# Performance work log

Measured on AMD Instinct MI355X. Metric: run time of the kernel, lower is better.

The kernel has to match this reference:

```python
import jax, jax.numpy as jnp
import numpy as np

N, D_IN, D_OUT, H, E = 8192, 1024, 1024, 1024, 8
EPS = 0.2
S_FACTOR = 5.0


def setup_inputs() -> dict:
    key = jax.random.key(0)
    k0, k1, k2, k3 = jax.random.split(key, 4)
    x = jax.random.normal(k0, (N, D_IN), jnp.float32)
    # selector Linear(nIn, E); weights scaled by sFactor as in SMoE.__init__
    Wsel = jax.random.normal(k1, (D_IN, E), jnp.float32) * (S_FACTOR / np.sqrt(D_IN))
    bsel = jnp.zeros((E,), jnp.float32)
    # stacked 2-layer MLP experts: Linear(D_IN,H) -> ReLU -> Linear(H,D_OUT)
    W1 = jax.random.normal(k2, (E, D_IN, H), jnp.float32) / np.sqrt(D_IN)
    b1 = jnp.zeros((E, H), jnp.float32)
    W2 = jax.random.normal(k3, (E, H, D_OUT), jnp.float32) / np.sqrt(H)
    b2 = jnp.zeros((E, D_OUT), jnp.float32)
    return {"x": x, "Wsel": Wsel, "bsel": bsel, "W1": W1, "b1": b1, "W2": W2, "b2": b2}


def _sparse_weights(weightMat):
    # sort experts per token, descending (torch.sort(..., 1, descending=True))
    order = jnp.argsort(-weightMat, axis=1)                # [N,E]
    topW = jnp.take_along_axis(weightMat, order, axis=1)
    cumW = jnp.cumsum(topW, axis=1)
    capped = jnp.minimum(cumW, 1.0 - EPS)
    sw_sorted = jax.nn.relu(capped - cumW + topW)          # sparse weights, sorted order
    # softCost (side-effect metric in the original; not returned by SMoE.forward)
    shifted = jnp.pad(sw_sorted[:, 1:], ((0, 0), (0, 1)))
    _soft_cost = jnp.sum(jnp.where(shifted > 0, 1.0, sw_sorted), axis=1)
    # faithful to torch.gather(sparse_weight, 1, index) in the source
    sw = jnp.take_along_axis(sw_sorted, order, axis=1)     # [N,E]
    return sw


def reference(x, Wsel, bsel, W1, b1, W2, b2):
    weightMat = jax.nn.softmax(x @ Wsel + bsel, axis=1)    # [N,E] selector
    sw = _sparse_weights(weightMat)                        # [N,E] sparse combine weights
    # dense (vectorized) expert dispatch: tokens with sw==0 contribute 0,
    # numerically identical to the gather/scatter_add loop in sparse_MoE
    h = jax.nn.relu(jnp.einsum('nd,edh->enh', x, W1) + b1[:, None, :])   # [E,N,H]
    y = jnp.einsum('enh,eho->eno', h, W2) + b2[:, None, :]               # [E,N,O]
    out = jnp.einsum('ne,eno->no', sw, y)                                # [N,O]
    return out
```

## Files before the change

kernel.cpp:

```cpp
#include <hip/hip_runtime.h>
#include <hip/hip_bf16.h>
#include <stdint.h>

#define N_TOK 8192
#define DIN   1024
#define DOUT  1024
#define HID   1024
#define NE    8
#define CAP   0.8f

typedef __attribute__((ext_vector_type(8))) short short8;
typedef __attribute__((ext_vector_type(4))) float floatx4;

__device__ __forceinline__ void async_load16(const void* g, void* l) {
  __builtin_amdgcn_global_load_lds(
      (const __attribute__((address_space(1))) void*)g,
      (__attribute__((address_space(3))) void*)l,
      16, 0, 0);
}

__device__ __forceinline__ unsigned short bf16_bits(float f) {
  return __builtin_bit_cast(unsigned short, __float2bfloat16(f));
}

__global__ __launch_bounds__(256) void selector_kernel(
    const float* __restrict__ x, const float* __restrict__ Wsel,
    const float* __restrict__ bsel,
    __hip_bfloat16* __restrict__ x_bf, float* __restrict__ sw,
    float4* __restrict__ out4)
{
  {
    const int base = blockIdx.x * 1024 + threadIdx.x;
    const float4 z4 = {0.f, 0.f, 0.f, 0.f};
#pragma unroll
    for (int r = 0; r < 4; r++) out4[base + r * 256] = z4;
  }

  const int lane = threadIdx.x & 63;
  const int wave = threadIdx.x >> 6;
  const int n = blockIdx.x * 4 + wave;
  const float4* xr4 = (const float4*)(x + (size_t)n * DIN);
  ushort4* xb4 = (ushort4*)(x_bf + (size_t)n * DIN);

  float acc[8];
#pragma unroll
  for (int e = 0; e < 8; e++) acc[e] = 0.f;

#pragma unroll
  for (int i = 0; i < 4; i++) {
    const int d4 = lane + i * 64;
    const float4 xv = xr4[d4];
    ushort4 p;
    p.x = bf16_bits(xv.x);
    p.y = bf16_bits(xv.y);
    p.z = bf16_bits(xv.z);
    p.w = bf16_bits(xv.w);
    xb4[d4] = p;
    const float xs[4] = {xv.x, xv.y, xv.z, xv.w};
#pragma unroll
    for (int q = 0; q < 4; q++) {
      const int d = d4 * 4 + q;
      const float4* wr = (const float4*)(Wsel + d * 8);
      const float4 wlo = wr[0], whi = wr[1];
      const float xv1 = xs[q];
      acc[0] += xv1 * wlo.x; acc[1] += xv1 * wlo.y;
      acc[2] += xv1 * wlo.z; acc[3] += xv1 * wlo.w;
      acc[4] += xv1 * whi.x; acc[5] += xv1 * whi.y;
      acc[6] += xv1 * whi.z; acc[7] += xv1 * whi.w;
    }
  }
#pragma unroll
  for (int off = 32; off >= 1; off >>= 1)
#pragma unroll
    for (int e = 0; e < 8; e++) acc[e] += __shfl_xor(acc[e], off);

  if (lane == 0) {
    float w[8];
    float mx = -1e30f;
#pragma unroll
    for (int e = 0; e < 8; e++) { w[e] = acc[e] + bsel[e]; mx = fmaxf(mx, w[e]); }
    float s = 0.f;
#pragma unroll
    for (int e = 0; e < 8; e++) { w[e] = expf(w[e] - mx); s += w[e]; }
    const float inv = 1.f / s;
#pragma unroll
    for (int e = 0; e < 8; e++) w[e] *= inv;

    float wsrt[8]; int ord[8];
    for (int k = 0; k < 8; k++) {
      const float v = w[k];
      int j = k;
      while (j > 0 && wsrt[j - 1] < v) { wsrt[j] = wsrt[j - 1]; ord[j] = ord[j - 1]; j--; }
      wsrt[j] = v; ord[j] = k;
    }
    float cum = 0.f, sws[8];
    for (int k = 0; k < 8; k++) {
      cum += wsrt[k];
      const float capped = fminf(cum, CAP);
      sws[k] = fmaxf(capped - cum + wsrt[k], 0.f);
    }
    for (int j = 0; j < 8; j++) sw[(size_t)n * 8 + j] = sws[ord[j]];
  }
}

__global__ __launch_bounds__(256) void compact_convert_kernel(
    const float* __restrict__ sw, int* __restrict__ idx, int* __restrict__ cnt,
    const float* __restrict__ W1, const float* __restrict__ W2,
    __hip_bfloat16* __restrict__ W1t, __hip_bfloat16* __restrict__ W2t)
{
  const int z = blockIdx.z;
  if (z == 16) {
    const int bid = blockIdx.x + 32 * blockIdx.y;
    if (bid >= 8) return;
    const int e = bid;
    const int t = threadIdx.x;
    const int lane = t & 63;
    const int wv = t >> 6;
    __shared__ int wave_base[4];
    __shared__ int chunk_total;
    int base = 0;
    for (int c = 0; c < 32; c++) {
      const int tok = c * 256 + t;
      const bool act = sw[(size_t)tok * 8 + e] > 0.f;
      const unsigned long long m = __ballot(act);
      const int before = __popcll(m & ((1ull << lane) - 1ull));
      if (lane == 0) wave_base[wv] = __popcll(m);
      __syncthreads();
      if (t == 0) {
        int s = 0;
        for (int w = 0; w < 4; w++) { const int v = wave_base[w]; wave_base[w] = s; s += v; }
        chunk_total = s;
      }
      __syncthreads();
      if (act) idx[e * N_TOK + base + wave_base[wv] + before] = tok;
      base += chunk_total;
      __syncthreads();
    }
    if (t == 0) cnt[e] = base;
    return;
  }

  __shared__ float tile[32][33];
  const float* src = (z & 8) ? W2 : W1;
  __hip_bfloat16* dst = (z & 8) ? W2t : W1t;
  const int e = z & 7;
  src += (size_t)e * 1024 * 1024;
  dst += (size_t)e * 1024 * 1024;
  const int R = blockIdx.y * 32, C = blockIdx.x * 32;
  const int c = threadIdx.x & 31, r0 = threadIdx.x >> 5;
#pragma unroll
  for (int p = 0; p < 4; p++) {
    const int r = r0 + p * 8;
    tile[r][c] = src[(size_t)(R + r) * 1024 + C + c];
  }
  __syncthreads();
#pragma unroll
  for (int p = 0; p < 4; p++) {
    const int r = r0 + p * 8;
    dst[(size_t)(C + r) * 1024 + R + c] = __float2bfloat16(tile[c][r]);
  }
}

#define BUFO (128 * 32)

template <int MODE>
__global__ __launch_bounds__(256, 2) void moe_gemm(
    const __hip_bfloat16* __restrict__ x_bf,
    __hip_bfloat16* __restrict__ hpool,
    const __hip_bfloat16* __restrict__ Wt,
    const float* __restrict__ biasAll,
    const float* __restrict__ sw,
    const int* __restrict__ idx, const int* __restrict__ cnt,
    float* __restrict__ out)
{
  const int lid = blockIdx.x + (blockIdx.y << 3) + (blockIdx.z << 9);
  const int xcd = lid & 7;
  const int s_ = lid >> 3;
  const int nb = s_ & 7;
  const int g  = s_ >> 3;
  const int e  = g & 7;
  const int mb = ((xcd - e) & 7) + ((g >> 3) << 3);

  const int count = cnt[e];
  const int m0 = mb * 128;
  if (m0 >= count) return;
  const int n0 = nb * 128;

  __shared__ __align__(16) __hip_bfloat16 sA[2 * BUFO];
  __shared__ __align__(16) __hip_bfloat16 sB[2 * BUFO];
  const int t = threadIdx.x;
  const int lane = t & 63;
  const int wave = t >> 6;
  const int wm = (wave & 1) * 64;
  const int wn = (wave >> 1) * 64;
  const int* idx_e = idx + e * N_TOK;
  const float* bias = biasAll + e * 1024;

  floatx4 acc[4][4];
#pragma unroll
  for (int i = 0; i < 4; i++)
#pragma unroll
    for (int j = 0; j < 4; j++) acc[i][j] = (floatx4){0.f, 0.f, 0.f, 0.f};

  const int sr = t >> 2;
  const int sc = (t & 3) * 8;
  const __hip_bfloat16* Ag0;
  const __hip_bfloat16* Ag1;
  if (MODE == 0) {
    const int t0 = idx_e[min(m0 + sr, count - 1)];
    const int t1 = idx_e[min(m0 + sr + 64, count - 1)];
    Ag0 = x_bf + (size_t)t0 * 1024 + sc;
    Ag1 = x_bf + (size_t)t1 * 1024 + sc;
  } else {
    const __hip_bfloat16* hp = hpool + (size_t)e * N_TOK * 1024;
    Ag0 = hp + (size_t)(m0 + sr) * 1024 + sc;
    Ag1 = hp + (size_t)(m0 + sr + 64) * 1024 + sc;
  }
  const __hip_bfloat16* Bg = Wt + (size_t)e * 1024 * 1024 + (size_t)(n0 + sr) * 1024 + sc;
  __hip_bfloat16* lA = &sA[sr * 32 + sc];
  __hip_bfloat16* lB = &sB[sr * 32 + sc];

  const int rf = lane & 15;
  const int k8 = (lane >> 4) * 8;
  const int roA = (wm + rf) * 32 + k8;
  const int roB = (wn + rf) * 32 + k8;

  async_load16(Ag0, lA);
  async_load16(Ag1, lA + 64 * 32);
  async_load16(Bg, lB);
  async_load16(Bg + (size_t)64 * 1024, lB + 64 * 32);
  __syncthreads();

#define STEP(KT, RB, WB)                                                        \
  {                                                                             \
    const int knext = ((KT) + 1) * 32;                                          \
    if (knext < 1024) {                                                         \
      async_load16(Ag0 + knext, lA + (WB) * BUFO);                              \
      async_load16(Ag1 + knext, lA + (WB) * BUFO + 64 * 32);                    \
      async_load16(Bg + knext, lB + (WB) * BUFO);                               \
      async_load16(Bg + (size_t)64 * 1024 + knext, lB + (WB) * BUFO + 64 * 32); \
    }                                                                           \
    const __hip_bfloat16* pA = &sA[(RB) * BUFO + roA];                          \
    const __hip_bfloat16* pB = &sB[(RB) * BUFO + roB];                          \
    short8 aF[4], bF[4];                                                        \
    _Pragma("unroll")                                                           \
    for (int i = 0; i < 4; i++) aF[i] = *(const short8*)(pA + i * 16 * 32);     \
    _Pragma("unroll")                                                           \
    for (int j = 0; j < 4; j++) bF[j] = *(const short8*)(pB + j * 16 * 32);     \
    _Pragma("unroll")                                                           \
    for (int i = 0; i < 4; i++)                                                 \
      _Pragma("unroll")                                                         \
      for (int j = 0; j < 4; j++)                                               \
        acc[i][j] = __builtin_amdgcn_mfma_f32_16x16x32_bf16(aF[i], bF[j],       \
                                                            acc[i][j], 0, 0, 0);\
    __syncthreads();                                                            \
  }

  for (int kt = 0; kt < 32; kt += 2) {
    STEP(kt, 0, 1);
    STEP(kt + 1, 1, 0);
  }
#undef STEP

  const int quad = lane >> 4;
  const int cn = lane & 15;
#pragma unroll
  for (int i = 0; i < 4; i++) {
#pragma unroll
    for (int r = 0; r < 4; r++) {
      const int gm = m0 + wm + i * 16 + quad * 4 + r;
      if (gm >= count) continue;
      int tok = 0; float swv = 0.f;
      if (MODE == 1) {
        tok = idx_e[gm];
        swv = sw[tok * 8 + e];
      }
#pragma unroll
      for (int j = 0; j < 4; j++) {
        const int gn = n0 + wn + j * 16 + cn;
        const float v = acc[i][j][r] + bias[gn];
        if (MODE == 0) {
          hpool[((size_t)e * N_TOK + gm) * 1024 + gn] = __float2bfloat16(fmaxf(v, 0.f));
        } else {
          unsafeAtomicAdd(&out[(size_t)tok * 1024 + gn], swv * v);
        }
      }
    }
  }
}

extern "C" void kernel_launch(void* const* d_in, const int* in_sizes, int n_in,
                              void* d_out, int out_size, void* d_ws, size_t ws_size,
                              hipStream_t stream) {
  const float* x    = (const float*)d_in[0];
  const float* Wsel = (const float*)d_in[1];
  const float* bsel = (const float*)d_in[2];
  const float* W1   = (const float*)d_in[3];
  const float* b1   = (const float*)d_in[4];
  const float* W2   = (const float*)d_in[5];
  const float* b2   = (const float*)d_in[6];
  float* out = (float*)d_out;

  char* ws = (char*)d_ws;
  __hip_bfloat16* x_bf = (__hip_bfloat16*)ws; ws += (size_t)N_TOK * DIN * 2;
  __hip_bfloat16* W1t  = (__hip_bfloat16*)ws; ws += (size_t)NE * DIN * HID * 2;
  __hip_bfloat16* W2t  = (__hip_bfloat16*)ws; ws += (size_t)NE * HID * DOUT * 2;
  float* sw            = (float*)ws;          ws += (size_t)N_TOK * NE * 4;
  int* idx             = (int*)ws;            ws += (size_t)NE * N_TOK * 4;
  int* cnt             = (int*)ws;            ws += 256;
  __hip_bfloat16* hpool = (__hip_bfloat16*)ws;

  selector_kernel<<<N_TOK / 4, 256, 0, stream>>>(x, Wsel, bsel, x_bf, sw,
                                                 (float4*)out);
  compact_convert_kernel<<<dim3(32, 32, 17), 256, 0, stream>>>(
      sw, idx, cnt, W1, W2, W1t, W2t);

  moe_gemm<0><<<dim3(HID / 128, N_TOK / 128, NE), 256, 0, stream>>>(
      x_bf, hpool, W1t, b1, sw, idx, cnt, out);
  moe_gemm<1><<<dim3(DOUT / 128, N_TOK / 128, NE), 256, 0, stream>>>(
      x_bf, hpool, W2t, b2, sw, idx, cnt, out);
}
```

Measured before the change: 322.0 us.

## Vectorize weight transpose-convert, widen compaction blocks, simplify GEMM block mapping

The weight transpose/convert kernel now uses 64x64 tiles with 1024 threads, float4 loads, and ushort4 bf16 stores, storing bf16 bits in shared memory. This cuts memory transactions and shared-memory traffic. The compaction step now processes 1024 tokens per iteration with 16 wave slots, so it needs fewer barrier rounds. The GEMM block index mapping drops the XCD-aware swizzle for a direct blockIdx mapping, which may hurt L2 locality across XCDs.

```diff
diff --git a/kernel.cpp b/kernel.cpp
--- a/kernel.cpp
+++ b/kernel.cpp
@@ -103,24 +103,26 @@
   }
 }
 
-__global__ __launch_bounds__(256) void compact_convert_kernel(
+__global__ __launch_bounds__(1024) void compact_convert_kernel(
     const float* __restrict__ sw, int* __restrict__ idx, int* __restrict__ cnt,
     const float* __restrict__ W1, const float* __restrict__ W2,
     __hip_bfloat16* __restrict__ W1t, __hip_bfloat16* __restrict__ W2t)
 {
   const int z = blockIdx.z;
+  const int t = threadIdx.x;
+
   if (z == 16) {
-    const int bid = blockIdx.x + 32 * blockIdx.y;
+    const int bid = blockIdx.x + 16 * blockIdx.y;
     if (bid >= 8) return;
     const int e = bid;
-    const int t = threadIdx.x;
     const int lane = t & 63;
     const int wv = t >> 6;
-    __shared__ int wave_base[4];
+    __shared__ int wave_base[16];
     __shared__ int chunk_total;
     int base = 0;
-    for (int c = 0; c < 32; c++) {
-      const int tok = c * 256 + t;
+#pragma unroll
+    for (int c = 0; c < 8; c++) {
+      const int tok = c * 1024 + t;
       const bool act = sw[(size_t)tok * 8 + e] > 0.f;
       const unsigned long long m = __ballot(act);
       const int before = __popcll(m & ((1ull << lane) - 1ull));
@@ -128,7 +130,7 @@
       __syncthreads();
       if (t == 0) {
         int s = 0;
-        for (int w = 0; w < 4; w++) { const int v = wave_base[w]; wave_base[w] = s; s += v; }
+        for (int w = 0; w < 16; w++) { const int v = wave_base[w]; wave_base[w] = s; s += v; }
         chunk_total = s;
       }
       __syncthreads();
@@ -140,24 +142,33 @@
     return;
   }
 
-  __shared__ float tile[32][33];
+  __shared__ unsigned short tile[64][65];
   const float* src = (z & 8) ? W2 : W1;
   __hip_bfloat16* dst = (z & 8) ? W2t : W1t;
   const int e = z & 7;
   src += (size_t)e * 1024 * 1024;
-  dst += (size_t)e * 1024 * 1024;
-  const int R = blockIdx.y * 32, C = blockIdx.x * 32;
-  const int c = threadIdx.x & 31, r0 = threadIdx.x >> 5;
-#pragma unroll
-  for (int p = 0; p < 4; p++) {
-    const int r = r0 + p * 8;
-    tile[r][c] = src[(size_t)(R + r) * 1024 + C + c];
+  unsigned short* dstu = (unsigned short*)dst + (size_t)e * 1024 * 1024;
+  const int R = blockIdx.y * 64, C = blockIdx.x * 64;
+
+  {
+    const int row = t >> 4;
+    const int col4 = t & 15;
+    const float4 v = *(const float4*)(src + (size_t)(R + row) * 1024 + C + col4 * 4);
+    tile[row][col4 * 4 + 0] = bf16_bits(v.x);
+    tile[row][col4 * 4 + 1] = bf16_bits(v.y);
+    tile[row][col4 * 4 + 2] = bf16_bits(v.z);
+    tile[row][col4 * 4 + 3] = bf16_bits(v.w);
   }
   __syncthreads();
-#pragma unroll
-  for (int p = 0; p < 4; p++) {
-    const int r = r0 + p * 8;
-    dst[(size_t)(C + r) * 1024 + R + c] = __float2bfloat16(tile[c][r]);
+  {
+    const int d = t >> 4;
+    const int j = t & 15;
+    ushort4 o;
+    o.x = tile[j * 4 + 0][d];
+    o.y = tile[j * 4 + 1][d];
+    o.z = tile[j * 4 + 2][d];
+    o.w = tile[j * 4 + 3][d];
+    *(ushort4*)(dstu + (size_t)(C + d) * 1024 + R + j * 4) = o;
   }
 }
 
@@ -173,18 +184,11 @@
     const int* __restrict__ idx, const int* __restrict__ cnt,
     float* __restrict__ out)
 {
-  const int lid = blockIdx.x + (blockIdx.y << 3) + (blockIdx.z << 9);
-  const int xcd = lid & 7;
-  const int s_ = lid >> 3;
-  const int nb = s_ & 7;
-  const int g  = s_ >> 3;
-  const int e  = g & 7;
-  const int mb = ((xcd - e) & 7) + ((g >> 3) << 3);
-
+  const int e = blockIdx.z;
   const int count = cnt[e];
-  const int m0 = mb * 128;
+  const int m0 = blockIdx.y * 128;
   if (m0 >= count) return;
-  const int n0 = nb * 128;
+  const int n0 = blockIdx.x * 128;
 
   __shared__ __align__(16) __hip_bfloat16 sA[2 * BUFO];
   __shared__ __align__(16) __hip_bfloat16 sB[2 * BUFO];
@@ -312,7 +316,7 @@
 
   selector_kernel<<<N_TOK / 4, 256, 0, stream>>>(x, Wsel, bsel, x_bf, sw,
                                                  (float4*)out);
-  compact_convert_kernel<<<dim3(32, 32, 17), 256, 0, stream>>>(
+  compact_convert_kernel<<<dim3(16, 16, 17), 1024, 0, stream>>>(
       sw, idx, cnt, W1, W2, W1t, W2t);
 
   moe_gemm<0><<<dim3(HID / 128, N_TOK / 128, NE), 256, 0, stream>>>(
```

New measurement: 315.1 us. 2.1% less time.
